# Optimization experiments

Hardware: AMD Instinct MI355X
Metric: run time of the kernel (lower is better)

Reference implementation:

```python
import jax, jax.numpy as jnp
import numpy as np

IN_DIM = 1024
HID = 256
OUT_DIM = 1000
NUM_BINS = 51
BATCH = 2048
N_LEGAL = 200


def setup_inputs() -> dict:
    key = jax.random.key(0)
    ks = jax.random.split(key, 12)
    s = lambda fan_in: 1.0 / np.sqrt(fan_in)
    u = lambda k, shp, b: jax.random.uniform(k, shp, jnp.float32, -b, b)
    return {
        "x": jax.random.normal(ks[0], (BATCH, IN_DIM), jnp.float32),
        # weights stored as [in, out] (math-equivalent to torch Linear)
        "w_in": u(ks[1], (IN_DIM, HID), s(IN_DIM)),
        "b_in": u(ks[2], (HID,), s(IN_DIM)),
        "w_ah": u(ks[3], (HID, HID), s(HID)),
        "b_ah": u(ks[4], (HID,), s(HID)),
        "w_ao": u(ks[5], (HID, OUT_DIM * NUM_BINS), s(HID)),
        "b_ao": u(ks[6], (OUT_DIM * NUM_BINS,), s(HID)),
        "w_vh": u(ks[7], (HID, HID), s(HID)),
        "b_vh": u(ks[8], (HID,), s(HID)),
        "w_vo": u(ks[9], (HID, NUM_BINS), s(HID)),
        "b_vo": u(ks[10], (NUM_BINS,), s(HID)),
        "v_range": jnp.linspace(-10.0, 10.0, NUM_BINS, dtype=jnp.float32),
        "possible_moves": jax.random.randint(ks[11], (BATCH, N_LEGAL), 0, OUT_DIM),
    }


def reference(x, w_in, b_in, w_ah, b_ah, w_ao, b_ao, w_vh, b_vh, w_vo, b_vo,
              v_range, possible_moves):
    B = x.shape[0]
    h = jax.nn.relu(x @ w_in + b_in)                       # [B, 256]
    adv_h = jax.nn.relu(h @ w_ah + b_ah)                   # [B, 256]
    val_h = jax.nn.relu(h @ w_vh + b_vh)                   # [B, 256]
    adv = (adv_h @ w_ao + b_ao).reshape(B, OUT_DIM, NUM_BINS)
    val = (val_h @ w_vo + b_vo).reshape(B, 1, NUM_BINS)
    q = val + adv - adv.mean(axis=1, keepdims=True)        # [B, A, bins]
    p = jnp.maximum(jax.nn.softmax(q, axis=2), 1e-5)       # softmax + clamp(min=1e-5)
    q_vals = jnp.sum(p * v_range, axis=2)                  # [B, A]
    # LegalSoftmax: per-row scatter of 1.0 at legal indices, vectorized
    mask = jnp.zeros((B, OUT_DIM), x.dtype).at[
        jnp.arange(B)[:, None], possible_moves].set(1.0)
    filtered = q_vals * mask
    # faithful to torch: any exact-zero entry (masked OR coincidental) -> -inf
    return jnp.where(filtered == 0, -jnp.inf, filtered)
```

## Files before the change

### kernel.cpp

```cpp
#include <hip/hip_runtime.h>
#include <cstdint>
#include <cstddef>

#define NB      2048
#define INDIM   1024
#define HID     256
#define NA      1000
#define BINS    51
#define NLEG    200
#define NPAIR   (NB*NLEG)
#define NBLK    256
#define PPB     (NPAIR/NBLK)

#define NEG_SENTINEL (-1.0e30f)

typedef float    f32x4  __attribute__((ext_vector_type(4)));
typedef __bf16   bf16x8 __attribute__((ext_vector_type(8)));
typedef unsigned short us8 __attribute__((ext_vector_type(8)));
typedef unsigned long long u64x2 __attribute__((ext_vector_type(2)));

__device__ __forceinline__ unsigned short f2bf(float f) {
  union { float f; unsigned u; } v; v.f = f;
  return (unsigned short)((v.u + 0x7FFFu + ((v.u >> 16) & 1u)) >> 16);
}
__device__ __forceinline__ float bf2f(unsigned short h) {
  union { unsigned u; float f; } v; v.u = ((unsigned)h) << 16;
  return v.f;
}
__device__ __forceinline__ bf16x8 as_bf(us8 v) { return __builtin_bit_cast(bf16x8, v); }
__device__ __forceinline__ int imin(int a, int b) { return a < b ? a : b; }

__device__ __forceinline__ unsigned f2fp8x4(float a, float b, float c, float d) {
  int v = 0;
  v = __builtin_amdgcn_cvt_pk_fp8_f32(a, b, v, false);
  v = __builtin_amdgcn_cvt_pk_fp8_f32(c, d, v, true);
  return (unsigned)v;
}
__device__ __forceinline__ unsigned char f2fp8(float f) {
  int v = __builtin_amdgcn_cvt_pk_fp8_f32(f, 0.f, 0, false);
  return (unsigned char)(v & 0xff);
}
__device__ __forceinline__ float fp82f(unsigned char u) {
  return __builtin_amdgcn_cvt_f32_fp8((int)u, 0);
}

__global__ __launch_bounds__(256) void k_phase1(
    const float* __restrict__ w_ao, unsigned char* __restrict__ wp8,
    float* __restrict__ wmean_acc,
    const float* __restrict__ w_in, const float* __restrict__ w_ah,
    const float* __restrict__ w_vh,
    unsigned short* __restrict__ w_inT, unsigned short* __restrict__ w_ahT,
    unsigned short* __restrict__ w_vhT,
    float* __restrict__ out, const int* __restrict__ pm,
    int* __restrict__ hist) {
  __shared__ __align__(16) char smem[26240];
  int b = blockIdx.x, tid = threadIdx.x;
  if (b < 1000) {
    unsigned char* st = (unsigned char*)smem;
    int s = b & 7, a0 = (b >> 3) * 8;
    const float* wbase = w_ao + (size_t)(s * 32) * (NA * BINS) + a0 * BINS;
    for (int i = tid; i < 32 * 102; i += 256) {
      int r = i / 102, c4 = i - r * 102;
      float4 f = *(const float4*)(wbase + (size_t)r * (NA * BINS) + c4 * 4);
      *(unsigned*)(st + r * 420 + c4 * 4) =
          f2fp8x4(f.x * 16.f, f.y * 16.f, f.z * 16.f, f.w * 16.f);
    }
    __syncthreads();
    for (int i = tid; i < 32 * 51; i += 256) {
      int r = i / 51, j = i - r * 51;
      float s8 = 0.f;
#pragma unroll
      for (int aL = 0; aL < 8; aL++) s8 += fp82f(st[r * 420 + aL * 51 + j]);
      atomicAdd(&wmean_acc[(size_t)(s * 32 + r) * BINS + j], s8);
    }
    int t4 = (tid >> 6) & 3, l = tid & 63;
    int col = t4 * 16 + (l & 15), kg = l >> 4;
    for (int aL = 0; aL < 8; aL++) {
      unsigned lo = 0, hi = 0;
      if (col < BINS) {
        const unsigned char* p0 = st + (kg * 8) * 420 + aL * 51 + col;
        lo = (unsigned)p0[0] | ((unsigned)p0[420] << 8) |
             ((unsigned)p0[840] << 16) | ((unsigned)p0[1260] << 24);
        hi = (unsigned)p0[1680] | ((unsigned)p0[2100] << 8) |
             ((unsigned)p0[2520] << 16) | ((unsigned)p0[2940] << 24);
      }
      size_t fg = ((size_t)(a0 + aL) * 8 + s) * 4 + t4;
      uint2 v; v.x = lo; v.y = hi;
      *(uint2*)(wp8 + fg * 512 + (size_t)l * 8) = v;
    }
  } else if (b < 1884) {
    int bb = b - 1000;
    if (bb < 384) {
      float (*tile)[33] = (float(*)[33])smem;
      const float* w; unsigned short* wT; int K, N, kt, nt;
      if (bb < 256)      { w = w_in; wT = w_inT; K = INDIM; N = HID; kt = bb & 31;        nt = bb >> 5; }
      else if (bb < 320) { w = w_ah; wT = w_ahT; K = HID;   N = HID; kt = (bb - 256) & 7; nt = (bb - 256) >> 3; }
      else               { w = w_vh; wT = w_vhT; K = HID;   N = HID; kt = (bb - 320) & 7; nt = (bb - 320) >> 3; }
      int k0 = kt * 32, n0 = nt * 32;
      int cr = tid >> 5, cc = tid & 31;
#pragma unroll
      for (int it = 0; it < 4; it++)
        tile[cr + it * 8][cc] = w[(size_t)(k0 + cr + it * 8) * N + n0 + cc];
      __syncthreads();
#pragma unroll
      for (int it = 0; it < 4; it++)
        wT[(size_t)(n0 + cr + it * 8) * K + k0 + cc] = f2bf(tile[cc][cr + it * 8]);
    } else {
      int base = (bb - 384) * 1024 + tid;
      float4 v = {NEG_SENTINEL, NEG_SENTINEL, NEG_SENTINEL, NEG_SENTINEL};
#pragma unroll
      for (int it = 0; it < 4; it++) ((float4*)out)[base + it * 256] = v;
    }
  } else {
    int* lh = (int*)smem;
    int blk = b - 1884;
    for (int i = tid; i < NA; i += 256) lh[i] = 0;
    __syncthreads();
    int base = blk * PPB;
    for (int i = tid; i < PPB; i += 256) atomicAdd(&lh[pm[base + i]], 1);
    __syncthreads();
    for (int a = tid; a < NA; a += 256) hist[a * NBLK + blk] = lh[a];
  }
}

__global__ __launch_bounds__(256) void k_phase2(
    int* __restrict__ hist, int* __restrict__ cnt,
    const float* __restrict__ w_vo, const float* __restrict__ wmean_acc,
    const float* __restrict__ b_vo, const float* __restrict__ b_ao,
    unsigned short* __restrict__ Wc, float* __restrict__ bias_c,
    const float* __restrict__ x, const unsigned short* __restrict__ w_inT,
    const float* __restrict__ b_in, unsigned short* __restrict__ h_bf) {
  int b = blockIdx.x, tid = threadIdx.x;
  if (b < 1000) {
    __shared__ int s[256];
    int a = b, t = tid;
    int v = hist[a * NBLK + t];
    s[t] = v;
    __syncthreads();
    for (int d = 1; d < 256; d <<= 1) {
      int u = (t >= d) ? s[t - d] : 0;
      __syncthreads();
      s[t] += u;
      __syncthreads();
    }
    hist[a * NBLK + t] = s[t] - v;
    if (t == 255) cnt[a] = s[255];
  } else if (b < 1064) {
    __shared__ float s[256];
    int n = b - 1000, t = tid;
    for (int k = t; k < 512; k += 256) {
      float v = 0.f;
      if (n < BINS)
        v = (k < 256) ? w_vo[(size_t)k * BINS + n]
                      : (-(0.001f / 16.f) * wmean_acc[(size_t)(k - 256) * BINS + n]);
      Wc[(size_t)n * 512 + k] = f2bf(v);
    }
    float acc = 0.f;
    if (n < BINS)
      for (int a = t; a < NA; a += 256) acc += b_ao[(size_t)a * BINS + n];
    s[t] = acc;
    __syncthreads();
    for (int d = 128; d > 0; d >>= 1) { if (t < d) s[t] += s[t + d]; __syncthreads(); }
    if (t == 0) bias_c[n] = (n < BINS) ? (b_vo[n] - 0.001f * s[0]) : 0.f;
  } else {
    int w = tid >> 6, l = tid & 63, la = l & 15, g = l >> 4;
    int idx = (b - 1064) * 4 + w;
    int m0 = (idx & 127) * 16, n0 = (idx >> 7) * 16;
    f32x4 acc = {0.f, 0.f, 0.f, 0.f};
    const us8* Bp = (const us8*)(w_inT + (size_t)(n0 + la) * INDIM) + g;
    const float* Ar = x + (size_t)(m0 + la) * INDIM + g * 8;
    for (int s = 0; s < INDIM; s += 32) {
      float4 f0 = *(const float4*)(Ar + s);
      float4 f1 = *(const float4*)(Ar + s + 4);
      us8 u;
      u[0] = f2bf(f0.x); u[1] = f2bf(f0.y); u[2] = f2bf(f0.z); u[3] = f2bf(f0.w);
      u[4] = f2bf(f1.x); u[5] = f2bf(f1.y); u[6] = f2bf(f1.z); u[7] = f2bf(f1.w);
      acc = __builtin_amdgcn_mfma_f32_16x16x32_bf16(as_bf(u), as_bf(Bp[s >> 3]),
                                                    acc, 0, 0, 0);
    }
    float bb = b_in[n0 + la];
#pragma unroll
    for (int r = 0; r < 4; r++) {
      float v = fmaxf(acc[r] + bb, 0.f);
      h_bf[(size_t)(m0 + g * 4 + r) * HID + n0 + la] = f2bf(v);
    }
  }
}

__global__ __launch_bounds__(256) void k_phase3(
    const int* __restrict__ cnt, int* __restrict__ off,
    const unsigned short* __restrict__ h,
    const unsigned short* __restrict__ wA, const float* __restrict__ bA,
    unsigned char* __restrict__ Aext8, unsigned short* __restrict__ advh_bf,
    const unsigned short* __restrict__ wV, const float* __restrict__ bV,
    unsigned short* __restrict__ oV) {
  int b = blockIdx.x, tid = threadIdx.x;
  if (b == 1024) {
    __shared__ int s[256];
    int t = tid, i0 = 4 * t;
    int v0 = (i0     < NA) ? cnt[i0]     : 0;
    int v1 = (i0 + 1 < NA) ? cnt[i0 + 1] : 0;
    int v2 = (i0 + 2 < NA) ? cnt[i0 + 2] : 0;
    int v3 = (i0 + 3 < NA) ? cnt[i0 + 3] : 0;
    int sum = v0 + v1 + v2 + v3;
    s[t] = sum;
    __syncthreads();
    for (int d = 1; d < 256; d <<= 1) {
      int u = (t >= d) ? s[t - d] : 0;
      __syncthreads();
      s[t] += u;
      __syncthreads();
    }
    int excl = s[t] - sum;
    if (i0     < NA) off[i0]     = excl;
    if (i0 + 1 < NA) off[i0 + 1] = excl + v0;
    if (i0 + 2 < NA) off[i0 + 2] = excl + v0 + v1;
    if (i0 + 3 < NA) off[i0 + 3] = excl + v0 + v1 + v2;
  } else {
    int w = tid >> 6, l = tid & 63, la = l & 15, g = l >> 4;
    int idx = b * 4 + w;
    int m0 = (idx & 127) * 16;
    int ny = idx >> 7;
    int second = ny >> 4;
    int n0 = (ny & 15) * 16;
    const unsigned short* BT = second ? wV : wA;
    const float* bias = second ? bV : bA;
    f32x4 acc = {0.f, 0.f, 0.f, 0.f};
    const us8* Bp = (const us8*)(BT + (size_t)(n0 + la) * HID) + g;
    const us8* Ap = (const us8*)(h + (size_t)(m0 + la) * HID) + g;
#pragma unroll
    for (int s = 0; s < 8; s++)
      acc = __builtin_amdgcn_mfma_f32_16x16x32_bf16(as_bf(Ap[s * 4]), as_bf(Bp[s * 4]),
                                                    acc, 0, 0, 0);
    float bb = bias[n0 + la];
#pragma unroll
    for (int r = 0; r < 4; r++) {
      float v = fmaxf(acc[r] + bb, 0.f);
      size_t o = (size_t)(m0 + g * 4 + r) * HID + n0 + la;
      if (second) {
        oV[o] = f2bf(v);
      } else {
        advh_bf[o] = f2bf(v);
        Aext8[o] = f2fp8(v);
      }
    }
  }
}

__global__ __launch_bounds__(256) void k_phase4(
    const int* __restrict__ pm, const int* __restrict__ off,
    const int* __restrict__ hist, int* __restrict__ rows,
    const unsigned short* __restrict__ valh, const unsigned short* __restrict__ advh,
    const unsigned short* __restrict__ Wc, const float* __restrict__ bias_c,
    unsigned short* __restrict__ cbuf) {
  int b = blockIdx.x, tid = threadIdx.x;
  if (b < 256) {
    __shared__ int lc[NA];
    __shared__ int lbase[NA];
    int blk = b, t = tid;
    for (int i = t; i < NA; i += 256) {
      lc[i] = 0;
      lbase[i] = off[i] + hist[i * NBLK + blk];
    }
    __syncthreads();
    int base = blk * PPB;
    for (int i = t; i < PPB; i += 256) {
      int a = pm[base + i];
      int r = atomicAdd(&lc[a], 1);
      rows[lbase[a] + r] = (base + i) / NLEG;
    }
  } else {
    int w = tid >> 6, l = tid & 63, la = l & 15, g = l >> 4;
    int idx = (b - 256) * 4 + w;
    int m0 = (idx & 127) * 16, n0 = (idx >> 7) * 16;
    f32x4 acc = {0.f, 0.f, 0.f, 0.f};
    const us8* Bp  = (const us8*)(Wc + (size_t)(n0 + la) * 512) + g;
    const us8* Ap1 = (const us8*)(valh + (size_t)(m0 + la) * HID) + g;
    const us8* Ap2 = (const us8*)(advh + (size_t)(m0 + la) * HID) + g;
#pragma unroll
    for (int s = 0; s < 8; s++)
      acc = __builtin_amdgcn_mfma_f32_16x16x32_bf16(as_bf(Ap1[s * 4]), as_bf(Bp[s * 4]),
                                                    acc, 0, 0, 0);
#pragma unroll
    for (int s = 0; s < 8; s++)
      acc = __builtin_amdgcn_mfma_f32_16x16x32_bf16(as_bf(Ap2[s * 4]), as_bf(Bp[(8 + s) * 4]),
                                                    acc, 0, 0, 0);
    float bb = bias_c[n0 + la];
#pragma unroll
    for (int r = 0; r < 4; r++)
      cbuf[(size_t)(m0 + g * 4 + r) * 64 + n0 + la] = f2bf(acc[r] + bb);
  }
}

__global__ __launch_bounds__(256) void k_main_mfma(
    const unsigned char* __restrict__ Aext8,
    const unsigned short* __restrict__ cbuf,
    const unsigned char* __restrict__ wp8,
    const float* __restrict__ b_ao,
    const float* __restrict__ v_range,
    const int* __restrict__ cnt, const int* __restrict__ off,
    const int* __restrict__ rows,
    float* __restrict__ out) {
  __shared__ __align__(16) long long sB8[2048];
  int bx = blockIdx.x;
  int a = (bx & 7) * 125 + (bx >> 3);
  int count = cnt[a];
  int ntiles = (count + 15) >> 4;
  if ((int)(blockIdx.y * 4) >= ntiles) return;
  int tid = threadIdx.x;
  const u64x2* wpa = (const u64x2*)(wp8 + (size_t)a * 16384);
  for (int i = tid; i < 1024; i += 256) ((u64x2*)sB8)[i] = wpa[i];
  __syncthreads();

  int w = tid >> 6, l = tid & 63, la = l & 15, g = l >> 4;
  int base = off[a];
  float vr[4], bao[4];
#pragma unroll
  for (int t = 0; t < 4; t++) {
    int bin = t * 16 + la;
    bool vb = bin < BINS;
    vr[t]  = vb ? v_range[bin] : 0.f;
    bao[t] = vb ? b_ao[(size_t)a * BINS + bin] : 0.f;
  }

  for (int tile = blockIdx.y * 4 + w; tile < ntiles; tile += 8) {
    int m16 = tile * 16;
    int rA = rows[base + imin(m16 + la, count - 1)];
    const long long* Ap = (const long long*)(Aext8 + (size_t)rA * HID) + g;
    const us8* Cp = (const us8*)(cbuf + (size_t)rA * 64) + g;
    f32x4 acc[4];
#pragma unroll
    for (int t = 0; t < 4; t++) acc[t] = (f32x4){0.f, 0.f, 0.f, 0.f};
#pragma unroll
    for (int s = 0; s < 8; s++) {
      long long a8 = Ap[s * 4];
#pragma unroll
      for (int t = 0; t < 4; t++)
        acc[t] = __builtin_amdgcn_mfma_f32_16x16x32_fp8_fp8(
            a8, sB8[(s * 4 + t) * 64 + l], acc[t], 0, 0, 0);
    }
    {
      us8 c0 = Cp[0], c1 = Cp[4];
#pragma unroll
      for (int t = 0; t < 4; t++) {
        int colg = t * 16 + la;
        us8 u0, u1;
#pragma unroll
        for (int j = 0; j < 8; j++) {
          u0[j] = (g * 8 + j == colg)      ? (unsigned short)0x4180 : (unsigned short)0;
          u1[j] = (g * 8 + j + 32 == colg) ? (unsigned short)0x4180 : (unsigned short)0;
        }
        acc[t] = __builtin_amdgcn_mfma_f32_16x16x32_bf16(as_bf(c0), as_bf(u0), acc[t], 0, 0, 0);
        acc[t] = __builtin_amdgcn_mfma_f32_16x16x32_bf16(as_bf(c1), as_bf(u1), acc[t], 0, 0, 0);
      }
    }
#pragma unroll
    for (int r = 0; r < 4; r++) {
      int gi = m16 + g * 4 + r;
      bool vrow = gi < count;
      int b = __shfl(rA, g * 4 + r, 16);
      float e[4];
      float S = 0.f;
#pragma unroll
      for (int t = 0; t < 4; t++) {
        int bin = t * 16 + la;
        float v = (bin < BINS) ? (acc[t][r] * 0.0625f + bao[t]) : -1.0e30f;
        e[t] = __expf(v);
        S += e[t];
      }
#pragma unroll
      for (int i = 1; i < 16; i <<= 1) S += __shfl_xor(S, i);
      float inv = 1.f / S;
      float qv = 0.f;
#pragma unroll
      for (int t = 0; t < 4; t++) {
        int bin = t * 16 + la;
        if (bin < BINS) qv = fmaf(fmaxf(e[t] * inv, 1e-5f), vr[t], qv);
      }
#pragma unroll
      for (int i = 1; i < 16; i <<= 1) qv += __shfl_xor(qv, i);
      if (vrow && la == 0)
        out[(size_t)b * NA + a] = (qv == 0.f) ? NEG_SENTINEL : qv;
    }
  }
}

extern "C" void kernel_launch(void* const* d_in, const int* in_sizes, int n_in,
                              void* d_out, int out_size, void* d_ws, size_t ws_size,
                              hipStream_t stream) {
  (void)in_sizes; (void)n_in; (void)out_size; (void)ws_size;
  const float* x     = (const float*)d_in[0];
  const float* w_in  = (const float*)d_in[1];
  const float* b_in  = (const float*)d_in[2];
  const float* w_ah  = (const float*)d_in[3];
  const float* b_ah  = (const float*)d_in[4];
  const float* w_ao  = (const float*)d_in[5];
  const float* b_ao  = (const float*)d_in[6];
  const float* w_vh  = (const float*)d_in[7];
  const float* b_vh  = (const float*)d_in[8];
  const float* w_vo  = (const float*)d_in[9];
  const float* b_vo  = (const float*)d_in[10];
  const float* v_rng = (const float*)d_in[11];
  const int*   pm    = (const int*)d_in[12];
  float* out = (float*)d_out;

  char* p = (char*)d_ws;
  unsigned char*  wp8     = (unsigned char*)p;  p += (size_t)NA * 32 * 512;
  unsigned char*  Aext8   = (unsigned char*)p;  p += (size_t)NB * HID;
  unsigned short* cbuf    = (unsigned short*)p; p += (size_t)NB * 64 * 2;
  unsigned short* h_bf    = (unsigned short*)p; p += (size_t)NB * HID * 2;
  unsigned short* advh_bf = (unsigned short*)p; p += (size_t)NB * HID * 2;
  unsigned short* valh_bf = (unsigned short*)p; p += (size_t)NB * HID * 2;
  unsigned short* w_inT   = (unsigned short*)p; p += (size_t)HID * INDIM * 2;
  unsigned short* w_ahT   = (unsigned short*)p; p += (size_t)HID * HID * 2;
  unsigned short* w_vhT   = (unsigned short*)p; p += (size_t)HID * HID * 2;
  unsigned short* Wc      = (unsigned short*)p; p += (size_t)64 * 512 * 2;
  float* bias_c = (float*)p; p += 64 * 4;
  float* wmean  = (float*)p; p += 13056 * 4;
  int* cnt  = (int*)p; p += NA * 4;
  int* off  = (int*)p; p += NA * 4;
  int* hist = (int*)p; p += (size_t)NA * NBLK * 4;
  int* rows = (int*)p; p += (size_t)NPAIR * 4 + 256;

  hipMemsetAsync(wmean, 0, 13056 * sizeof(float), stream);

  k_phase1<<<2140, 256, 0, stream>>>(w_ao, wp8, wmean, w_in, w_ah, w_vh,
                                     w_inT, w_ahT, w_vhT, out, pm, hist);
  k_phase2<<<1576, 256, 0, stream>>>(hist, cnt, w_vo, wmean, b_vo, b_ao,
                                     Wc, bias_c, x, w_inT, b_in, h_bf);
  k_phase3<<<1025, 256, 0, stream>>>(cnt, off, h_bf, w_ahT, b_ah, Aext8,
                                     advh_bf, w_vhT, b_vh, valh_bf);
  k_phase4<<<384, 256, 0, stream>>>(pm, off, hist, rows, valh_bf, advh_bf,
                                    Wc, bias_c, cbuf);
  k_main_mfma<<<dim3(1000, 2), 256, 0, stream>>>(Aext8, cbuf, wp8, b_ao, v_rng,
                                                 cnt, off, rows, out);
}
```

Measured before the change: 221.2 us.

## Rebalance phase kernels, pre-convert x to bf16, and transpose main MFMA epilogue

```diff
diff --git a/kernel.cpp b/kernel.cpp
--- a/kernel.cpp
+++ b/kernel.cpp
@@ -17,6 +17,7 @@
 typedef float    f32x4  __attribute__((ext_vector_type(4)));
 typedef __bf16   bf16x8 __attribute__((ext_vector_type(8)));
 typedef unsigned short us8 __attribute__((ext_vector_type(8)));
+typedef unsigned short us4 __attribute__((ext_vector_type(4)));
 typedef unsigned long long u64x2 __attribute__((ext_vector_type(2)));
 
 __device__ __forceinline__ unsigned short f2bf(float f) {
@@ -52,7 +53,8 @@
     unsigned short* __restrict__ w_inT, unsigned short* __restrict__ w_ahT,
     unsigned short* __restrict__ w_vhT,
     float* __restrict__ out, const int* __restrict__ pm,
-    int* __restrict__ hist) {
+    int* __restrict__ hist, int* __restrict__ cnt,
+    const float* __restrict__ x, unsigned short* __restrict__ x_bf) {
   __shared__ __align__(16) char smem[26240];
   int b = blockIdx.x, tid = threadIdx.x;
   if (b < 1000) {
@@ -111,7 +113,7 @@
 #pragma unroll
       for (int it = 0; it < 4; it++) ((float4*)out)[base + it * 256] = v;
     }
-  } else {
+  } else if (b < 2140) {
     int* lh = (int*)smem;
     int blk = b - 1884;
     for (int i = tid; i < NA; i += 256) lh[i] = 0;
@@ -119,17 +121,32 @@
     int base = blk * PPB;
     for (int i = tid; i < PPB; i += 256) atomicAdd(&lh[pm[base + i]], 1);
     __syncthreads();
-    for (int a = tid; a < NA; a += 256) hist[a * NBLK + blk] = lh[a];
+    for (int a = tid; a < NA; a += 256) {
+      int v = lh[a];
+      hist[a * NBLK + blk] = v;
+      if (v) atomicAdd(&cnt[a], v);
+    }
+  } else {
+    int bb = b - 2140;
+    int base4 = bb * 1024 + tid;
+#pragma unroll
+    for (int it = 0; it < 4; it++) {
+      float4 v = ((const float4*)x)[base4 + it * 256];
+      us4 o;
+      o[0] = f2bf(v.x); o[1] = f2bf(v.y); o[2] = f2bf(v.z); o[3] = f2bf(v.w);
+      ((us4*)x_bf)[base4 + it * 256] = o;
+    }
   }
 }
 
 __global__ __launch_bounds__(256) void k_phase2(
-    int* __restrict__ hist, int* __restrict__ cnt,
+    int* __restrict__ hist, const int* __restrict__ cnt,
     const float* __restrict__ w_vo, const float* __restrict__ wmean_acc,
     const float* __restrict__ b_vo, const float* __restrict__ b_ao,
     unsigned short* __restrict__ Wc, float* __restrict__ bias_c,
-    const float* __restrict__ x, const unsigned short* __restrict__ w_inT,
-    const float* __restrict__ b_in, unsigned short* __restrict__ h_bf) {
+    const unsigned short* __restrict__ x_bf, const unsigned short* __restrict__ w_inT,
+    const float* __restrict__ b_in, unsigned short* __restrict__ h_bf,
+    int* __restrict__ off) {
   int b = blockIdx.x, tid = threadIdx.x;
   if (b < 1000) {
     __shared__ int s[256];
@@ -144,7 +161,6 @@
       __syncthreads();
     }
     hist[a * NBLK + t] = s[t] - v;
-    if (t == 255) cnt[a] = s[255];
   } else if (b < 1064) {
     __shared__ float s[256];
     int n = b - 1000, t = tid;
@@ -162,40 +178,24 @@
     __syncthreads();
     for (int d = 128; d > 0; d >>= 1) { if (t < d) s[t] += s[t + d]; __syncthreads(); }
     if (t == 0) bias_c[n] = (n < BINS) ? (b_vo[n] - 0.001f * s[0]) : 0.f;
-  } else {
+  } else if (b < 1576) {
     int w = tid >> 6, l = tid & 63, la = l & 15, g = l >> 4;
     int idx = (b - 1064) * 4 + w;
     int m0 = (idx & 127) * 16, n0 = (idx >> 7) * 16;
     f32x4 acc = {0.f, 0.f, 0.f, 0.f};
     const us8* Bp = (const us8*)(w_inT + (size_t)(n0 + la) * INDIM) + g;
-    const float* Ar = x + (size_t)(m0 + la) * INDIM + g * 8;
-    for (int s = 0; s < INDIM; s += 32) {
-      float4 f0 = *(const float4*)(Ar + s);
-      float4 f1 = *(const float4*)(Ar + s + 4);
-      us8 u;
-      u[0] = f2bf(f0.x); u[1] = f2bf(f0.y); u[2] = f2bf(f0.z); u[3] = f2bf(f0.w);
-      u[4] = f2bf(f1.x); u[5] = f2bf(f1.y); u[6] = f2bf(f1.z); u[7] = f2bf(f1.w);
-      acc = __builtin_amdgcn_mfma_f32_16x16x32_bf16(as_bf(u), as_bf(Bp[s >> 3]),
+    const us8* Ap = (const us8*)(x_bf + (size_t)(m0 + la) * INDIM) + g;
+#pragma unroll 8
+    for (int s = 0; s < 32; s++)
+      acc = __builtin_amdgcn_mfma_f32_16x16x32_bf16(as_bf(Ap[s * 4]), as_bf(Bp[s * 4]),
                                                     acc, 0, 0, 0);
-    }
     float bb = b_in[n0 + la];
 #pragma unroll
     for (int r = 0; r < 4; r++) {
       float v = fmaxf(acc[r] + bb, 0.f);
       h_bf[(size_t)(m0 + g * 4 + r) * HID + n0 + la] = f2bf(v);
     }
-  }
-}
-
-__global__ __launch_bounds__(256) void k_phase3(
-    const int* __restrict__ cnt, int* __restrict__ off,
-    const unsigned short* __restrict__ h,
-    const unsigned short* __restrict__ wA, const float* __restrict__ bA,
-    unsigned char* __restrict__ Aext8, unsigned short* __restrict__ advh_bf,
-    const unsigned short* __restrict__ wV, const float* __restrict__ bV,
-    unsigned short* __restrict__ oV) {
-  int b = blockIdx.x, tid = threadIdx.x;
-  if (b == 1024) {
+  } else {
     __shared__ int s[256];
     int t = tid, i0 = 4 * t;
     int v0 = (i0     < NA) ? cnt[i0]     : 0;
@@ -216,7 +216,19 @@
     if (i0 + 1 < NA) off[i0 + 1] = excl + v0;
     if (i0 + 2 < NA) off[i0 + 2] = excl + v0 + v1;
     if (i0 + 3 < NA) off[i0 + 3] = excl + v0 + v1 + v2;
-  } else {
+  }
+}
+
+__global__ __launch_bounds__(256) void k_phase3(
+    const unsigned short* __restrict__ h,
+    const unsigned short* __restrict__ wA, const float* __restrict__ bA,
+    unsigned char* __restrict__ Aext8, unsigned short* __restrict__ advh_bf,
+    const unsigned short* __restrict__ wV, const float* __restrict__ bV,
+    unsigned short* __restrict__ oV,
+    const int* __restrict__ pm, const int* __restrict__ off,
+    const int* __restrict__ hist, int* __restrict__ rows) {
+  int b = blockIdx.x, tid = threadIdx.x;
+  if (b < 1024) {
     int w = tid >> 6, l = tid & 63, la = l & 15, g = l >> 4;
     int idx = b * 4 + w;
     int m0 = (idx & 127) * 16;
@@ -244,20 +256,10 @@
         Aext8[o] = f2fp8(v);
       }
     }
-  }
-}
-
-__global__ __launch_bounds__(256) void k_phase4(
-    const int* __restrict__ pm, const int* __restrict__ off,
-    const int* __restrict__ hist, int* __restrict__ rows,
-    const unsigned short* __restrict__ valh, const unsigned short* __restrict__ advh,
-    const unsigned short* __restrict__ Wc, const float* __restrict__ bias_c,
-    unsigned short* __restrict__ cbuf) {
-  int b = blockIdx.x, tid = threadIdx.x;
-  if (b < 256) {
+  } else {
     __shared__ int lc[NA];
     __shared__ int lbase[NA];
-    int blk = b, t = tid;
+    int blk = b - 1024, t = tid;
     for (int i = t; i < NA; i += 256) {
       lc[i] = 0;
       lbase[i] = off[i] + hist[i * NBLK + blk];
@@ -269,27 +271,33 @@
       int r = atomicAdd(&lc[a], 1);
       rows[lbase[a] + r] = (base + i) / NLEG;
     }
-  } else {
-    int w = tid >> 6, l = tid & 63, la = l & 15, g = l >> 4;
-    int idx = (b - 256) * 4 + w;
-    int m0 = (idx & 127) * 16, n0 = (idx >> 7) * 16;
-    f32x4 acc = {0.f, 0.f, 0.f, 0.f};
-    const us8* Bp  = (const us8*)(Wc + (size_t)(n0 + la) * 512) + g;
-    const us8* Ap1 = (const us8*)(valh + (size_t)(m0 + la) * HID) + g;
-    const us8* Ap2 = (const us8*)(advh + (size_t)(m0 + la) * HID) + g;
-#pragma unroll
-    for (int s = 0; s < 8; s++)
-      acc = __builtin_amdgcn_mfma_f32_16x16x32_bf16(as_bf(Ap1[s * 4]), as_bf(Bp[s * 4]),
-                                                    acc, 0, 0, 0);
-#pragma unroll
-    for (int s = 0; s < 8; s++)
-      acc = __builtin_amdgcn_mfma_f32_16x16x32_bf16(as_bf(Ap2[s * 4]), as_bf(Bp[(8 + s) * 4]),
-                                                    acc, 0, 0, 0);
-    float bb = bias_c[n0 + la];
-#pragma unroll
-    for (int r = 0; r < 4; r++)
-      cbuf[(size_t)(m0 + g * 4 + r) * 64 + n0 + la] = f2bf(acc[r] + bb);
   }
+}
+
+__global__ __launch_bounds__(256) void k_phase4(
+    const unsigned short* __restrict__ valh, const unsigned short* __restrict__ advh,
+    const unsigned short* __restrict__ Wc, const float* __restrict__ bias_c,
+    unsigned short* __restrict__ cbuf) {
+  int b = blockIdx.x, tid = threadIdx.x;
+  int w = tid >> 6, l = tid & 63, la = l & 15, g = l >> 4;
+  int idx = b * 4 + w;
+  int m0 = (idx & 127) * 16, n0 = (idx >> 7) * 16;
+  f32x4 acc = {0.f, 0.f, 0.f, 0.f};
+  const us8* Bp  = (const us8*)(Wc + (size_t)(n0 + la) * 512) + g;
+  const us8* Ap1 = (const us8*)(valh + (size_t)(m0 + la) * HID) + g;
+  const us8* Ap2 = (const us8*)(advh + (size_t)(m0 + la) * HID) + g;
+#pragma unroll
+  for (int s = 0; s < 8; s++)
+    acc = __builtin_amdgcn_mfma_f32_16x16x32_bf16(as_bf(Ap1[s * 4]), as_bf(Bp[s * 4]),
+                                                  acc, 0, 0, 0);
+#pragma unroll
+  for (int s = 0; s < 8; s++)
+    acc = __builtin_amdgcn_mfma_f32_16x16x32_bf16(as_bf(Ap2[s * 4]), as_bf(Bp[(8 + s) * 4]),
+                                                  acc, 0, 0, 0);
+  float bb = bias_c[n0 + la];
+#pragma unroll
+  for (int r = 0; r < 4; r++)
+    cbuf[(size_t)(m0 + g * 4 + r) * 64 + n0 + la] = f2bf(acc[r] + bb);
 }
 
 __global__ __launch_bounds__(256) void k_main_mfma(
@@ -314,18 +322,28 @@
 
   int w = tid >> 6, l = tid & 63, la = l & 15, g = l >> 4;
   int base = off[a];
-  float vr[4], bao[4];
-#pragma unroll
-  for (int t = 0; t < 4; t++) {
-    int bin = t * 16 + la;
-    bool vb = bin < BINS;
-    vr[t]  = vb ? v_range[bin] : 0.f;
-    bao[t] = vb ? b_ao[(size_t)a * BINS + bin] : 0.f;
+
+  float vr[4][4], bao[4][4];
+#pragma unroll
+  for (int t = 0; t < 4; t++)
+#pragma unroll
+    for (int r = 0; r < 4; r++) {
+      int bin = t * 16 + g * 4 + r;
+      bool vb = bin < BINS;
+      vr[t][r]  = vb ? v_range[bin] : 0.f;
+      bao[t][r] = vb ? b_ao[(size_t)a * BINS + bin] : NEG_SENTINEL;
+    }
+
+  us8 id0, id1;
+#pragma unroll
+  for (int j = 0; j < 8; j++) {
+    id0[j] = (g * 8 + j == la)      ? (unsigned short)0x4180 : (unsigned short)0;
+    id1[j] = (g * 8 + j == la + 16) ? (unsigned short)0x4180 : (unsigned short)0;
   }
 
   for (int tile = blockIdx.y * 4 + w; tile < ntiles; tile += 8) {
-    int m16 = tile * 16;
-    int rA = rows[base + imin(m16 + la, count - 1)];
+    int gi = tile * 16 + la;
+    int rA = rows[base + imin(gi, count - 1)];
     const long long* Ap = (const long long*)(Aext8 + (size_t)rA * HID) + g;
     const us8* Cp = (const us8*)(cbuf + (size_t)rA * 64) + g;
     f32x4 acc[4];
@@ -337,51 +355,38 @@
 #pragma unroll
       for (int t = 0; t < 4; t++)
         acc[t] = __builtin_amdgcn_mfma_f32_16x16x32_fp8_fp8(
-            a8, sB8[(s * 4 + t) * 64 + l], acc[t], 0, 0, 0);
+            sB8[(s * 4 + t) * 64 + l], a8, acc[t], 0, 0, 0);
     }
     {
       us8 c0 = Cp[0], c1 = Cp[4];
-#pragma unroll
-      for (int t = 0; t < 4; t++) {
-        int colg = t * 16 + la;
-        us8 u0, u1;
-#pragma unroll
-        for (int j = 0; j < 8; j++) {
-          u0[j] = (g * 8 + j == colg)      ? (unsigned short)0x4180 : (unsigned short)0;
-          u1[j] = (g * 8 + j + 32 == colg) ? (unsigned short)0x4180 : (unsigned short)0;
-        }
-        acc[t] = __builtin_amdgcn_mfma_f32_16x16x32_bf16(as_bf(c0), as_bf(u0), acc[t], 0, 0, 0);
-        acc[t] = __builtin_amdgcn_mfma_f32_16x16x32_bf16(as_bf(c1), as_bf(u1), acc[t], 0, 0, 0);
+      acc[0] = __builtin_amdgcn_mfma_f32_16x16x32_bf16(as_bf(id0), as_bf(c0), acc[0], 0, 0, 0);
+      acc[1] = __builtin_amdgcn_mfma_f32_16x16x32_bf16(as_bf(id1), as_bf(c0), acc[1], 0, 0, 0);
+      acc[2] = __builtin_amdgcn_mfma_f32_16x16x32_bf16(as_bf(id0), as_bf(c1), acc[2], 0, 0, 0);
+      acc[3] = __builtin_amdgcn_mfma_f32_16x16x32_bf16(as_bf(id1), as_bf(c1), acc[3], 0, 0, 0);
+    }
+    float e[4][4], S = 0.f;
+#pragma unroll
+    for (int t = 0; t < 4; t++)
+#pragma unroll
+      for (int r = 0; r < 4; r++) {
+        float q = fmaf(acc[t][r], 0.0625f, bao[t][r]);
+        float ev = __expf(q);
+        e[t][r] = ev;
+        S += ev;
       }
-    }
-#pragma unroll
-    for (int r = 0; r < 4; r++) {
-      int gi = m16 + g * 4 + r;
-      bool vrow = gi < count;
-      int b = __shfl(rA, g * 4 + r, 16);
-      float e[4];
-      float S = 0.f;
-#pragma unroll
-      for (int t = 0; t < 4; t++) {
-        int bin = t * 16 + la;
-        float v = (bin < BINS) ? (acc[t][r] * 0.0625f + bao[t]) : -1.0e30f;
-        e[t] = __expf(v);
-        S += e[t];
-      }
-#pragma unroll
-      for (int i = 1; i < 16; i <<= 1) S += __shfl_xor(S, i);
-      float inv = 1.f / S;
-      float qv = 0.f;
-#pragma unroll
-      for (int t = 0; t < 4; t++) {
-        int bin = t * 16 + la;
-        if (bin < BINS) qv = fmaf(fmaxf(e[t] * inv, 1e-5f), vr[t], qv);
-      }
-#pragma unroll
-      for (int i = 1; i < 16; i <<= 1) qv += __shfl_xor(qv, i);
-      if (vrow && la == 0)
-        out[(size_t)b * NA + a] = (qv == 0.f) ? NEG_SENTINEL : qv;
-    }
+    S += __shfl_xor(S, 16);
+    S += __shfl_xor(S, 32);
+    float inv = 1.f / S;
+    float qv = 0.f;
+#pragma unroll
+    for (int t = 0; t < 4; t++)
+#pragma unroll
+      for (int r = 0; r < 4; r++)
+        qv = fmaf(fmaxf(e[t][r] * inv, 1e-5f), vr[t][r], qv);
+    qv += __shfl_xor(qv, 16);
+    qv += __shfl_xor(qv, 32);
+    if (g == 0 && gi < count)
+      out[(size_t)rA * NA + a] = (qv == 0.f) ? NEG_SENTINEL : qv;
   }
 }
 
@@ -415,6 +420,7 @@
   unsigned short* w_ahT   = (unsigned short*)p; p += (size_t)HID * HID * 2;
   unsigned short* w_vhT   = (unsigned short*)p; p += (size_t)HID * HID * 2;
   unsigned short* Wc      = (unsigned short*)p; p += (size_t)64 * 512 * 2;
+  unsigned short* x_bf    = (unsigned short*)p; p += (size_t)NB * INDIM * 2;
   float* bias_c = (float*)p; p += 64 * 4;
   float* wmean  = (float*)p; p += 13056 * 4;
   int* cnt  = (int*)p; p += NA * 4;
@@ -422,16 +428,16 @@
   int* hist = (int*)p; p += (size_t)NA * NBLK * 4;
   int* rows = (int*)p; p += (size_t)NPAIR * 4 + 256;
 
-  hipMemsetAsync(wmean, 0, 13056 * sizeof(float), stream);
-
-  k_phase1<<<2140, 256, 0, stream>>>(w_ao, wp8, wmean, w_in, w_ah, w_vh,
-                                     w_inT, w_ahT, w_vhT, out, pm, hist);
-  k_phase2<<<1576, 256, 0, stream>>>(hist, cnt, w_vo, wmean, b_vo, b_ao,
-                                     Wc, bias_c, x, w_inT, b_in, h_bf);
-  k_phase3<<<1025, 256, 0, stream>>>(cnt, off, h_bf, w_ahT, b_ah, Aext8,
-                                     advh_bf, w_vhT, b_vh, valh_bf);
-  k_phase4<<<384, 256, 0, stream>>>(pm, off, hist, rows, valh_bf, advh_bf,
-                                    Wc, bias_c, cbuf);
+  hipMemsetAsync(wmean, 0, (13056 + NA) * sizeof(float), stream);
+
+  k_phase1<<<2652, 256, 0, stream>>>(w_ao, wp8, wmean, w_in, w_ah, w_vh,
+                                     w_inT, w_ahT, w_vhT, out, pm, hist, cnt,
+                                     x, x_bf);
+  k_phase2<<<1577, 256, 0, stream>>>(hist, cnt, w_vo, wmean, b_vo, b_ao,
+                                     Wc, bias_c, x_bf, w_inT, b_in, h_bf, off);
+  k_phase3<<<1280, 256, 0, stream>>>(h_bf, w_ahT, b_ah, Aext8, advh_bf,
+                                     w_vhT, b_vh, valh_bf, pm, off, hist, rows);
+  k_phase4<<<128, 256, 0, stream>>>(valh_bf, advh_bf, Wc, bias_c, cbuf);
   k_main_mfma<<<dim3(1000, 2), 256, 0, stream>>>(Aext8, cbuf, wp8, b_ao, v_rng,
                                                  cnt, off, rows, out);
 }
```

Measured after the change: 207.6 us. 1.07x faster.
